# Optimization experiments

Hardware: AMD Instinct MI355X
Metric: run time of the kernel (lower is better)

The kernel has to match this reference:

```python
import jax, jax.numpy as jnp
import numpy as np
import math

DIM = 1024
HEADS = 16
HEAD_DIM = DIM // HEADS
ROT = min(HEAD_DIM, 32)  # rotary_dim
B, S = 2, 1024


def setup_inputs() -> dict:
    key = jax.random.key(0)
    ks = jax.random.split(key, 32)
    lin = lambda k: jax.random.normal(k, (DIM, DIM), jnp.float32) * 0.02
    bias = lambda k: jax.random.normal(k, (DIM,), jnp.float32) * 0.01
    inp = {
        'real': jax.random.normal(ks[0], (B, S, DIM), jnp.float32),
        'imag': jax.random.normal(ks[1], (B, S, DIM), jnp.float32),
        'Wq_r': lin(ks[2]), 'bq_r': bias(ks[3]),
        'Wk_r': lin(ks[4]), 'bk_r': bias(ks[5]),
        'Wv_r': lin(ks[6]), 'bv_r': bias(ks[7]),
        'Wq_i': lin(ks[8]), 'bq_i': bias(ks[9]),
        'Wk_i': lin(ks[10]), 'bk_i': bias(ks[11]),
        'Wv_i': lin(ks[12]), 'bv_i': bias(ks[13]),
        'Wo_r': lin(ks[14]), 'bo_r': bias(ks[15]),
        'Wo_i': lin(ks[16]), 'bo_i': bias(ks[17]),
        'phase_shifts': jax.random.normal(ks[18], (HEADS, HEAD_DIM), jnp.float32) * 0.02,
        'ent': jnp.eye(HEADS, dtype=jnp.float32) + jax.random.normal(ks[19], (HEADS, HEADS), jnp.float32) * 0.01,
        'rot_freqs': (10000.0 ** (-jnp.arange(0, ROT, 2, dtype=jnp.float32) / ROT)),
        'strength': jnp.ones((1,), jnp.float32),
        'temp': jnp.ones((1,), jnp.float32),
    }
    return inp


def _fwd(real, imag, Wq_r, bq_r, Wk_r, bk_r, Wv_r, bv_r,
         Wq_i, bq_i, Wk_i, bk_i, Wv_i, bv_i,
         Wo_r, bo_r, Wo_i, bo_i,
         phase_shifts, ent, rot_freqs, strength, temp):
    b, s, _ = real.shape
    to_heads = lambda t: t.reshape(b, s, HEADS, HEAD_DIM).transpose(0, 2, 1, 3)  # bhsd
    lin = lambda x, W, bb: x @ W + bb

    q_r = to_heads(lin(real, Wq_r, bq_r))
    k_r = to_heads(lin(real, Wk_r, bk_r))
    v_r = to_heads(lin(real, Wv_r, bv_r))
    q_i = to_heads(lin(imag, Wq_i, bq_i))
    k_i = to_heads(lin(imag, Wk_i, bk_i))
    v_i = to_heads(lin(imag, Wv_i, bv_i))

    # rotary on first ROT dims (pairwise rotation)
    pos = jnp.arange(s, dtype=jnp.float32)
    emb = pos[:, None] * rot_freqs[None, :]           # [S, ROT/2]
    cos = jnp.cos(emb)[None, None]                    # [1,1,S,ROT/2]
    sin = jnp.sin(emb)[None, None]

    def rope(t):
        tr = t[..., :ROT].reshape(b, HEADS, s, ROT // 2, 2)
        r0 = tr[..., 0] * cos - tr[..., 1] * sin
        r1 = tr[..., 1] * cos + tr[..., 0] * sin
        rr = jnp.stack([r0, r1], axis=-1).reshape(b, HEADS, s, ROT)
        return jnp.concatenate([rr, t[..., ROT:]], axis=-1)

    q_r, k_r = rope(q_r), rope(k_r)
    q_i, k_i = rope(q_i), rope(k_i)

    # entanglement mixing across heads
    mix = lambda t: jnp.einsum('bhsd,hx->bxsd', t, ent)
    q_r, q_i, k_r, k_i = mix(q_r), mix(q_i), mix(k_r), mix(k_i)

    # per-head phase shift (complex rotation)
    pc = jnp.cos(phase_shifts)[None, :, None, :]      # [1,H,1,D]
    ps = jnp.sin(phase_shifts)[None, :, None, :]
    q_r, q_i = q_r * pc - q_i * ps, q_r * ps + q_i * pc
    k_r, k_i = k_r * pc - k_i * ps, k_r * ps + k_i * pc

    scale = 1.0 / math.sqrt(HEAD_DIM)
    attn_r = (jnp.einsum('bhqd,bhkd->bhqk', q_r, k_r) + jnp.einsum('bhqd,bhkd->bhqk', q_i, k_i)) * scale
    attn_i = (jnp.einsum('bhqd,bhkd->bhqk', q_i, k_r) - jnp.einsum('bhqd,bhkd->bhqk', q_r, k_i)) * scale
    attn_mag = jnp.sqrt(attn_r ** 2 + attn_i ** 2 + 1e-6)

    causal = jnp.triu(jnp.ones((s, s), dtype=bool), k=1)[None, None]
    attn_mag = jnp.where(causal, -jnp.inf, attn_mag)

    t = jnp.maximum(temp, 0.01)
    g = jax.nn.sigmoid(strength)
    attn = jax.nn.softmax(attn_mag * g / t, axis=-1)

    out_r = jnp.einsum('bhqk,bhkd->bhqd', attn, v_r).transpose(0, 2, 1, 3).reshape(b, s, DIM)
    out_i = jnp.einsum('bhqk,bhkd->bhqd', attn, v_i).transpose(0, 2, 1, 3).reshape(b, s, DIM)
    return lin(out_r, Wo_r, bo_r), lin(out_i, Wo_i, bo_i)


def reference(real, imag, Wq_r, bq_r, Wk_r, bk_r, Wv_r, bv_r,
              Wq_i, bq_i, Wk_i, bk_i, Wv_i, bv_i,
              Wo_r, bo_r, Wo_i, bo_i,
              phase_shifts, ent, rot_freqs, strength, temp):
    return _fwd(real, imag, Wq_r, bq_r, Wk_r, bk_r, Wv_r, bv_r,
                Wq_i, bq_i, Wk_i, bk_i, Wv_i, bv_i,
                Wo_r, bo_r, Wo_i, bo_i,
                phase_shifts, ent, rot_freqs, strength, temp)
```

## Files before the change

kernel.cpp:

```cpp
#include <hip/hip_runtime.h>
#include <stdint.h>

typedef unsigned short u16;
typedef __bf16 bf16x8 __attribute__((ext_vector_type(8)));
typedef float f32x4 __attribute__((ext_vector_type(4)));
typedef unsigned int u32x4 __attribute__((ext_vector_type(4)));

__device__ __forceinline__ u16 f2bf(float f) {
  uint32_t u = __float_as_uint(f);
  u += 0x7FFFu + ((u >> 16) & 1u);
  return (u16)(u >> 16);
}
__device__ __forceinline__ float bf2f(u16 h) {
  return __uint_as_float(((uint32_t)h) << 16);
}
__device__ __forceinline__ float fsqrt(float x) {
  float r; asm("v_sqrt_f32 %0, %1" : "=v"(r) : "v"(x)); return r;
}
__device__ __forceinline__ void gld16(const void* g, void* lds) {
  __builtin_amdgcn_global_load_lds(
      (const __attribute__((address_space(1))) uint32_t*)g,
      (__attribute__((address_space(3))) uint32_t*)lds, 16, 0, 0);
}
__device__ __forceinline__ f32x4 mfma16(u32x4 a, u32x4 b, f32x4 c) {
  return __builtin_amdgcn_mfma_f32_16x16x32_bf16(
      __builtin_bit_cast(bf16x8, a), __builtin_bit_cast(bf16x8, b), c, 0, 0, 0);
}

__global__ __launch_bounds__(256) void tables_kernel(const float* __restrict__ rotf,
                                                     const float* __restrict__ phase,
                                                     float* __restrict__ T) {
  int id = blockIdx.x * 256 + threadIdx.x;
  if (id < 16384) {
    int s = id >> 4, jj = id & 15;
    float sn, cs;
    sincosf((float)s * rotf[jj], &sn, &cs);
    T[id] = cs;
    T[16384 + id] = sn;
  } else if (id < 16384 + 1024) {
    int p = id - 16384;
    float sn, cs;
    sincosf(phase[p], &sn, &cs);
    T[32768 + p] = cs;
    T[33792 + p] = sn;
  }
}

__global__ __launch_bounds__(256) void convx_kernel(const float* __restrict__ real,
                                                    const float* __restrict__ imag,
                                                    u16* __restrict__ Xr,
                                                    u16* __restrict__ Xi) {
  int u = blockIdx.x * 256 + threadIdx.x;
  int a = u >> 18;
  int r = u & 262143;
  int m = r >> 7, slot = r & 127;
  const float* src = (a ? imag : real) + (size_t)m * 1024 + slot * 8;
  int slot2 = (slot & ~7) | ((slot ^ m) & 7);
  u16* dst = (a ? Xi : Xr) + (size_t)m * 1024 + slot2 * 8;
  f32x4 v0 = *(const f32x4*)(src);
  f32x4 v1 = *(const f32x4*)(src + 4);
  union { u16 h[8]; u32x4 v; } o;
#pragma unroll
  for (int e = 0; e < 4; ++e) { o.h[e] = f2bf(v0[e]); o.h[4 + e] = f2bf(v1[e]); }
  *(u32x4*)dst = o.v;
}

__global__ __launch_bounds__(256) void convw_kernel(
    const float* __restrict__ w0, const float* __restrict__ w1,
    const float* __restrict__ w2, const float* __restrict__ w3,
    const float* __restrict__ w4, const float* __restrict__ w5,
    const float* __restrict__ w6, const float* __restrict__ w7,
    u16* __restrict__ WtAll) {
  __shared__ float Lt[64][65];
  int z = blockIdx.z;
  const float* W = (z == 0) ? w0 : (z == 1) ? w1 : (z == 2) ? w2 : (z == 3) ? w3
                 : (z == 4) ? w4 : (z == 5) ? w5 : (z == 6) ? w6 : w7;
  u16* Wt = WtAll + (size_t)z * (1024 * 1024);
  int tid = threadIdx.x;
  int n0 = blockIdx.x * 64, k0 = blockIdx.y * 64;
#pragma unroll
  for (int it = 0; it < 4; ++it) {
    int idx = it * 256 + tid;
    int kr = idx >> 4, nc = (idx & 15) * 4;
    f32x4 v = *(const f32x4*)(W + (size_t)(k0 + kr) * 1024 + n0 + nc);
#pragma unroll
    for (int e = 0; e < 4; ++e) Lt[kr][nc + e] = v[e];
  }
  __syncthreads();
#pragma unroll
  for (int it = 0; it < 2; ++it) {
    int idx = it * 256 + tid;
    int nr = idx >> 3, sl = idx & 7;
    union { u16 h[8]; u32x4 v; } o;
#pragma unroll
    for (int e = 0; e < 8; ++e) o.h[e] = f2bf(Lt[sl * 8 + e][nr]);
    int sl2 = sl ^ (nr & 7);
    *(u32x4*)(Wt + (size_t)(n0 + nr) * 1024 + k0 + sl2 * 8) = o.v;
  }
}

__device__ __forceinline__ void gemm128(const u16* __restrict__ A, const u16* __restrict__ W,
                                        const float* __restrict__ bias,
                                        u16* __restrict__ outB, float* __restrict__ outF) {
  __shared__ __align__(16) u16 As[2][128 * 64];
  __shared__ __align__(16) u16 Bs[2][128 * 64];
  int tid = threadIdx.x, l = tid & 63, w = tid >> 6;
  int lr = l & 15, lh = l >> 4;
  int m0 = blockIdx.y * 128, n0 = blockIdx.x * 128;
  int wr = w >> 1, wc = w & 1;
  f32x4 acc[4][4];
#pragma unroll
  for (int mi = 0; mi < 4; ++mi)
#pragma unroll
    for (int ni = 0; ni < 4; ++ni) acc[mi][ni] = f32x4{0.f, 0.f, 0.f, 0.f};

  const u16* aA = A + (size_t)(m0 + w * 8 + (l >> 3)) * 1024 + (l & 7) * 8;
  const u16* aW = W + (size_t)(n0 + w * 8 + (l >> 3)) * 1024 + (l & 7) * 8;
  int ldoff = w * 1024 + l * 16;

  auto stage = [&](int buf, int kt) {
    const u16* pA = aA + kt * 64;
    const u16* pW = aW + kt * 64;
    char* dA = (char*)As[buf] + ldoff;
    char* dB = (char*)Bs[buf] + ldoff;
#pragma unroll
    for (int c = 0; c < 4; ++c) {
      gld16(pA + c * 32768, dA + c * 4096);
      gld16(pW + c * 32768, dB + c * 4096);
    }
  };

  stage(0, 0);

  for (int kt = 0; kt < 16; ++kt) {
    int cur = kt & 1;
    if (kt < 15) {
      stage(cur ^ 1, kt + 1);
      asm volatile("s_waitcnt vmcnt(8)" ::: "memory");
    } else {
      asm volatile("s_waitcnt vmcnt(0)" ::: "memory");
    }
    __builtin_amdgcn_sched_barrier(0);
    asm volatile("s_barrier" ::: "memory");

    const char* cA = (const char*)As[cur];
    const char* cB = (const char*)Bs[cur];
#pragma unroll
    for (int kk = 0; kk < 2; ++kk) {
      u32x4 af[4], bf[4];
#pragma unroll
      for (int mi = 0; mi < 4; ++mi) {
        int row = wr * 64 + mi * 16 + lr;
        af[mi] = *(const u32x4*)(cA + row * 128 +
                                 ((kk * 64 + lh * 16) ^ ((row & 7) << 4)));
      }
#pragma unroll
      for (int ni = 0; ni < 4; ++ni) {
        int row = wc * 64 + ni * 16 + lr;
        bf[ni] = *(const u32x4*)(cB + row * 128 +
                                 ((kk * 64 + lh * 16) ^ ((row & 7) << 4)));
      }
#pragma unroll
      for (int mi = 0; mi < 4; ++mi)
#pragma unroll
        for (int ni = 0; ni < 4; ++ni)
          acc[mi][ni] = mfma16(af[mi], bf[ni], acc[mi][ni]);
    }
    asm volatile("s_barrier" ::: "memory");
  }
#pragma unroll
  for (int ni = 0; ni < 4; ++ni) {
    int col = n0 + wc * 64 + ni * 16 + lr;
    float bv = bias[col];
#pragma unroll
    for (int mi = 0; mi < 4; ++mi)
#pragma unroll
      for (int rr = 0; rr < 4; ++rr) {
        int row = m0 + wr * 64 + mi * 16 + 4 * lh + rr;
        float v = acc[mi][ni][rr] + bv;
        if (outF) outF[(size_t)row * 1024 + col] = v;
        else      outB[(size_t)row * 1024 + col] = f2bf(v);
      }
  }
}

__global__ __launch_bounds__(256) void gemm_proj_kernel(
    const u16* __restrict__ Xr, const u16* __restrict__ Xi, const u16* __restrict__ Wt,
    const float* b0, const float* b1, const float* b2,
    const float* b3, const float* b4, const float* b5,
    u16* __restrict__ qkv) {
  int z = blockIdx.z;
  const u16* A = (z < 3) ? Xr : Xi;
  const u16* W = Wt + (size_t)z * (1024 * 1024);
  const float* bias = (z == 0) ? b0 : (z == 1) ? b1 : (z == 2) ? b2
                    : (z == 3) ? b3 : (z == 4) ? b4 : b5;
  u16* out = qkv + (size_t)z * (2048 * 1024);
  gemm128(A, W, bias, out, nullptr);
}

__global__ __launch_bounds__(256) void gemm_out_kernel(
    const u16* __restrict__ O, const u16* __restrict__ Wt2,
    const float* br, const float* bi, float* __restrict__ dout) {
  int z = blockIdx.z;
  gemm128(O + (size_t)z * (2048 * 1024), Wt2 + (size_t)z * (1024 * 1024),
          z ? bi : br, nullptr, dout + (size_t)z * (2048 * 1024));
}

__global__ __launch_bounds__(256) void transform_kernel(
    const u16* __restrict__ qkv, const float* __restrict__ ent,
    const float* __restrict__ T,
    u16* __restrict__ Qr, u16* __restrict__ Qi, u16* __restrict__ Kr,
    u16* __restrict__ Ki, u16* __restrict__ Vr, u16* __restrict__ Vi) {
  __shared__ float Lqr[16][65], Lqi[16][65], Lkr[16][65], Lki[16][65];
  __shared__ float sent[256];
  int tid = threadIdx.x;
  int bs = blockIdx.x;
  int b = bs >> 10, s = bs & 1023;
  sent[tid] = ent[tid];
  const u16* qr_raw = qkv;
  const u16* kr_raw = qkv + (size_t)1 * 2048 * 1024;
  const u16* vr_raw = qkv + (size_t)2 * 2048 * 1024;
  const u16* qi_raw = qkv + (size_t)3 * 2048 * 1024;
  const u16* ki_raw = qkv + (size_t)4 * 2048 * 1024;
  const u16* vi_raw = qkv + (size_t)5 * 2048 * 1024;
  size_t rowoff = (size_t)bs * 1024;
#pragma unroll
  for (int it = 0; it < 2; ++it) {
    int u = it * 256 + tid;
    int hh = u >> 5, j = u & 31;
    int base = hh * 64 + 2 * j;
    uint32_t aqr = *(const uint32_t*)(qr_raw + rowoff + base);
    uint32_t aqi = *(const uint32_t*)(qi_raw + rowoff + base);
    uint32_t akr = *(const uint32_t*)(kr_raw + rowoff + base);
    uint32_t aki = *(const uint32_t*)(ki_raw + rowoff + base);
    float qr0 = bf2f((u16)aqr), qr1 = bf2f((u16)(aqr >> 16));
    float qi0 = bf2f((u16)aqi), qi1 = bf2f((u16)(aqi >> 16));
    float kr0 = bf2f((u16)akr), kr1 = bf2f((u16)(akr >> 16));
    float ki0 = bf2f((u16)aki), ki1 = bf2f((u16)(aki >> 16));
    if (j < 16) {
      float cs = T[s * 16 + j];
      float sn = T[16384 + s * 16 + j];
      float t0;
      t0 = qr0; qr0 = t0 * cs - qr1 * sn; qr1 = qr1 * cs + t0 * sn;
      t0 = qi0; qi0 = t0 * cs - qi1 * sn; qi1 = qi1 * cs + t0 * sn;
      t0 = kr0; kr0 = t0 * cs - kr1 * sn; kr1 = kr1 * cs + t0 * sn;
      t0 = ki0; ki0 = t0 * cs - ki1 * sn; ki1 = ki1 * cs + t0 * sn;
    }
    int d0 = 2 * j;
    Lqr[hh][d0] = qr0; Lqr[hh][d0 + 1] = qr1;
    Lqi[hh][d0] = qi0; Lqi[hh][d0 + 1] = qi1;
    Lkr[hh][d0] = kr0; Lkr[hh][d0 + 1] = kr1;
    Lki[hh][d0] = ki0; Lki[hh][d0 + 1] = ki1;
  }
  __syncthreads();
#pragma unroll
  for (int it = 0; it < 4; ++it) {
    int u = it * 256 + tid;
    int x = u >> 6, d = u & 63;
    float mqr = 0.f, mqi = 0.f, mkr = 0.f, mki = 0.f;
#pragma unroll
    for (int hh = 0; hh < 16; ++hh) {
      float e = sent[hh * 16 + x];
      mqr += Lqr[hh][d] * e; mqi += Lqi[hh][d] * e;
      mkr += Lkr[hh][d] * e; mki += Lki[hh][d] * e;
    }
    float pc_ = T[32768 + x * 64 + d];
    float ps_ = T[33792 + x * 64 + d];
    float oqr = (mqr * pc_ - mqi * ps_) * 0.125f;
    float oqi = (mqr * ps_ + mqi * pc_) * 0.125f;
    float okr = mkr * pc_ - mki * ps_;
    float oki = mkr * ps_ + mki * pc_;
    size_t obase = ((size_t)(b * 16 + x) * 1024 + s) * 64;
    Qr[obase + d] = f2bf(oqr);
    Qi[obase + d] = f2bf(oqi);
    int dsw = (d & 7) | ((((d >> 3) ^ s) & 7) << 3);
    Kr[obase + dsw] = f2bf(okr);
    Ki[obase + dsw] = f2bf(oki);
  }
  {
    int u = tid;
    int comp = u >> 7, hh = (u >> 3) & 15, sl = u & 7;
    const u16* src = comp ? vi_raw : vr_raw;
    u16* dst = comp ? Vi : Vr;
    u32x4 vv = *(const u32x4*)(src + rowoff + hh * 64 + sl * 8);
    *(u32x4*)(dst + ((size_t)(b * 16 + hh) * 1024 + s) * 64 + sl * 8) = vv;
  }
}

__global__ __launch_bounds__(256) void transv_kernel(const u16* __restrict__ Vr,
                                                     const u16* __restrict__ Vi,
                                                     u16* __restrict__ VTr,
                                                     u16* __restrict__ VTi) {
  int bid = blockIdx.x;
  int comp = bid >> 9, bh = (bid >> 4) & 31, t = bid & 15;
  const u16* src = (comp ? Vi : Vr) + ((size_t)bh * 1024 + t * 64) * 64;
  u16* dst = (comp ? VTi : VTr) + (size_t)bh * 65536;
  __shared__ __align__(16) u16 Lt[64][72];
  int tid = threadIdx.x;
#pragma unroll
  for (int it = 0; it < 2; ++it) {
    int i = it * 256 + tid;
    int r = i >> 3, sl = i & 7;
    *(u32x4*)(&Lt[r][sl * 8]) = *(const u32x4*)(src + r * 64 + sl * 8);
  }
  __syncthreads();
#pragma unroll
  for (int it = 0; it < 2; ++it) {
    int i = it * 256 + tid;
    int d = i >> 3, sl = i & 7;
    union { u16 h[8]; u32x4 v; } o;
#pragma unroll
    for (int e = 0; e < 8; ++e) o.h[e] = Lt[sl * 8 + e][d];
    int sl2 = sl ^ (d & 7);
    *(u32x4*)(dst + (size_t)d * 1024 + t * 64 + sl2 * 8) = o.v;
  }
}

__global__ __launch_bounds__(256) void attn_kernel(
    const u16* __restrict__ Qr, const u16* __restrict__ Qi,
    const u16* __restrict__ Kr, const u16* __restrict__ Ki,
    const u16* __restrict__ VTr, const u16* __restrict__ VTi,
    const float* __restrict__ strength, const float* __restrict__ temp,
    u16* __restrict__ por0, u16* __restrict__ por1,
    u16* __restrict__ por2, u16* __restrict__ por3,
    u16* __restrict__ poi0, u16* __restrict__ poi1,
    u16* __restrict__ poi2, u16* __restrict__ poi3,
    float* __restrict__ Pm, float* __restrict__ Pl) {
  __shared__ __align__(16) u16 smem[20480];
  char* sb = (char*)smem;
  const int PO = 32768;
  int tid = threadIdx.x, l = tid & 63, w = tid >> 6;
  int lr = l & 15, lh = l >> 4;
  int id = blockIdx.x;
  int x = id & 7, j = id >> 3;
  int bh = x + 8 * (j & 3);
  int cc = j >> 2;
  int qb, sp;
  if (cc < 16)      { qb = 15 - (cc >> 2); sp = cc & 3; }
  else if (cc < 28) { int r = cc - 16; int q3 = r / 3; qb = 11 - q3; sp = r - 3 * q3; }
  else if (cc < 36) { int r = cc - 28; qb = 7 - (r >> 1); sp = r & 1; }
  else              { qb = 39 - cc; sp = 0; }
  int q0 = qb * 64;
  int t0 = sp * 4, t1 = min(qb + 1, t0 + 4);
  int b = bh >> 4; (void)b;
  u16* POr = (sp == 0) ? por0 : (sp == 1) ? por1 : (sp == 2) ? por2 : por3;
  u16* POi = (sp == 0) ? poi0 : (sp == 1) ? poi1 : (sp == 2) ? poi2 : poi3;

  float g = 1.f / (1.f + __expf(-strength[0]));
  float tt = fmaxf(temp[0], 0.01f);
  float gt = g / tt;

  size_t qbase = ((size_t)bh * 1024 + q0 + w * 16 + lr) * 64 + lh * 8;
  u32x4 qrF[2], qiF[2], nqrF[2];
#pragma unroll
  for (int kk = 0; kk < 2; ++kk) {
    qrF[kk] = *(const u32x4*)(Qr + qbase + kk * 32);
    qiF[kk] = *(const u32x4*)(Qi + qbase + kk * 32);
    nqrF[kk] = qrF[kk] ^ 0x80008000u;
  }
  f32x4 o_r[4], o_i[4];
#pragma unroll
  for (int n = 0; n < 4; ++n) { o_r[n] = f32x4{0,0,0,0}; o_i[n] = f32x4{0,0,0,0}; }
  float m_run[4], l_run[4];
#pragma unroll
  for (int rr = 0; rr < 4; ++rr) { m_run[rr] = -__builtin_inff(); l_run[rr] = 0.f; }

  const u16* gK = ((w == 1) ? Ki : Kr) + ((size_t)bh * 1024 + t0 * 64) * 64 + l * 8;
  char* ldK = sb + (w == 1 ? 8192 : 0);
  const u16* gV = ((w == 3) ? VTi : VTr) + (size_t)bh * 65536 + t0 * 64 +
                  (l >> 3) * 1024 + (l & 7) * 8;
  char* ldV = sb + (w == 3 ? 24576 : 16384);

  for (int t = t0; t < t1; ++t) {
    if (w < 2) {
#pragma unroll
      for (int c = 0; c < 8; ++c) gld16(gK + c * 512, ldK + c * 1024);
      gK += 4096;
    } else {
#pragma unroll
      for (int c = 0; c < 8; ++c) gld16(gV + c * 8192, ldV + c * 1024);
      gV += 64;
    }
    __syncthreads();

    f32x4 sr[4], si[4];
#pragma unroll
    for (int n = 0; n < 4; ++n) { sr[n] = f32x4{0,0,0,0}; si[n] = f32x4{0,0,0,0}; }
#pragma unroll
    for (int kk = 0; kk < 2; ++kk) {
#pragma unroll
      for (int n = 0; n < 4; ++n) {
        int kv = n * 16 + lr;
        int xoff = (kk * 64 + lh * 16) ^ ((kv & 7) << 4);
        u32x4 fkr = *(const u32x4*)(sb + kv * 128 + xoff);
        u32x4 fki = *(const u32x4*)(sb + 8192 + kv * 128 + xoff);
        sr[n] = mfma16(qrF[kk], fkr, sr[n]);
        sr[n] = mfma16(qiF[kk], fki, sr[n]);
        si[n] = mfma16(qiF[kk], fkr, si[n]);
        si[n] = mfma16(nqrF[kk], fki, si[n]);
      }
    }

    float pl_[4][4], pm[4];
#pragma unroll
    for (int rr = 0; rr < 4; ++rr) pm[rr] = -__builtin_inff();
    bool diag = (t == qb);
#pragma unroll
    for (int n = 0; n < 4; ++n)
#pragma unroll
      for (int rr = 0; rr < 4; ++rr) {
        float a = sr[n][rr], ci = si[n][rr];
        float mag = fsqrt(a * a + ci * ci + 1e-6f) * gt;
        if (diag) {
          if (n * 16 + lr > w * 16 + 4 * lh + rr) mag = -__builtin_inff();
        }
        pl_[n][rr] = mag;
        pm[rr] = fmaxf(pm[rr], mag);
      }
#pragma unroll
    for (int mk = 1; mk <= 8; mk <<= 1)
#pragma unroll
      for (int rr = 0; rr < 4; ++rr)
        pm[rr] = fmaxf(pm[rr], __shfl_xor(pm[rr], mk));

    bool defer = true;
#pragma unroll
    for (int rr = 0; rr < 4; ++rr) defer = defer && (pm[rr] - m_run[rr] <= 8.f);
    bool noresc = __all(defer ? 1 : 0);
    float fr[4];
    if (!noresc) {
#pragma unroll
      for (int rr = 0; rr < 4; ++rr) {
        float mnew = fmaxf(m_run[rr], pm[rr]);
        fr[rr] = __expf(m_run[rr] - mnew);
        m_run[rr] = mnew;
      }
    }
    float rs[4];
#pragma unroll
    for (int rr = 0; rr < 4; ++rr) rs[rr] = 0.f;
#pragma unroll
    for (int n = 0; n < 4; ++n)
#pragma unroll
      for (int rr = 0; rr < 4; ++rr) {
        float p = __expf(pl_[n][rr] - m_run[rr]);
        pl_[n][rr] = p;
        rs[rr] += p;
      }
#pragma unroll
    for (int mk = 1; mk <= 8; mk <<= 1)
#pragma unroll
      for (int rr = 0; rr < 4; ++rr)
        rs[rr] += __shfl_xor(rs[rr], mk);
    if (!noresc) {
#pragma unroll
      for (int rr = 0; rr < 4; ++rr) l_run[rr] = l_run[rr] * fr[rr] + rs[rr];
#pragma unroll
      for (int n = 0; n < 4; ++n)
#pragma unroll
        for (int rr = 0; rr < 4; ++rr) { o_r[n][rr] *= fr[rr]; o_i[n][rr] *= fr[rr]; }
    } else {
#pragma unroll
      for (int rr = 0; rr < 4; ++rr) l_run[rr] += rs[rr];
    }

    char* pw = sb + PO + w * 2048;
#pragma unroll
    for (int n = 0; n < 4; ++n)
#pragma unroll
      for (int rr = 0; rr < 4; ++rr) {
        int row = 4 * lh + rr, col = n * 16 + lr;
        int by = row * 128 + ((col & 7) * 2) + ((((col >> 3) ^ row) & 7) << 4);
        *(u16*)(pw + by) = f2bf(pl_[n][rr]);
      }
    u32x4 pf[2];
#pragma unroll
    for (int kk = 0; kk < 2; ++kk)
      pf[kk] = *(const u32x4*)(pw + lr * 128 + ((kk * 64 + lh * 16) ^ ((lr & 7) << 4)));
#pragma unroll
    for (int kk = 0; kk < 2; ++kk)
#pragma unroll
      for (int n = 0; n < 4; ++n) {
        int dl = n * 16 + lr;
        int xoff = (kk * 64 + lh * 16) ^ ((dl & 7) << 4);
        u32x4 fvr = *(const u32x4*)(sb + 16384 + dl * 128 + xoff);
        u32x4 fvi = *(const u32x4*)(sb + 24576 + dl * 128 + xoff);
        o_r[n] = mfma16(pf[kk], fvr, o_r[n]);
        o_i[n] = mfma16(pf[kk], fvi, o_i[n]);
      }
    __syncthreads();
  }

  size_t pbase = ((size_t)bh * 1024 + q0 + w * 16 + 4 * lh) * 64;
#pragma unroll
  for (int n = 0; n < 4; ++n)
#pragma unroll
    for (int rr = 0; rr < 4; ++rr) {
      POr[pbase + rr * 64 + n * 16 + lr] = f2bf(o_r[n][rr]);
      POi[pbase + rr * 64 + n * 16 + lr] = f2bf(o_i[n][rr]);
    }
  if (lr == 0) {
    size_t mbase = (size_t)sp * 32768 + (size_t)bh * 1024 + q0 + w * 16 + 4 * lh;
#pragma unroll
    for (int rr = 0; rr < 4; ++rr) {
      Pm[mbase + rr] = m_run[rr];
      Pl[mbase + rr] = l_run[rr];
    }
  }
}

__global__ __launch_bounds__(256) void combine_kernel(
    const u16* __restrict__ por0, const u16* __restrict__ por1,
    const u16* __restrict__ por2, const u16* __restrict__ por3,
    const u16* __restrict__ poi0, const u16* __restrict__ poi1,
    const u16* __restrict__ poi2, const u16* __restrict__ poi3,
    const float* __restrict__ Pm, const float* __restrict__ Pl,
    u16* __restrict__ Or, u16* __restrict__ Oi) {
  int bid = blockIdx.x;
  int bh = bid >> 4, rg = bid & 15;
  int b = bh >> 4, h = bh & 15;
  int ns = (rg >> 2) + 1;
  int tid = threadIdx.x;
  int row = tid >> 2, q = tid & 3;
  int s = rg * 64 + row;
  size_t ro = (size_t)bh * 1024 + s;
  const u16* PR[4] = {por0, por1, por2, por3};
  const u16* PI[4] = {poi0, poi1, poi2, poi3};
  float msp[4], lsp[4], csw[4];
  float M = -__builtin_inff();
#pragma unroll
  for (int sp = 0; sp < 4; ++sp) {
    if (sp < ns) {
      msp[sp] = Pm[ro + (size_t)sp * 32768];
      lsp[sp] = Pl[ro + (size_t)sp * 32768];
      M = fmaxf(M, msp[sp]);
    }
  }
  float lt = 0.f;
#pragma unroll
  for (int sp = 0; sp < 4; ++sp) {
    if (sp < ns) { csw[sp] = __expf(msp[sp] - M); lt += lsp[sp] * csw[sp]; }
    else csw[sp] = 0.f;
  }
  float inv = 1.f / lt;
#pragma unroll
  for (int sp = 0; sp < 4; ++sp) csw[sp] *= inv;
  size_t obase = ro * 64;
#pragma unroll
  for (int g = 0; g < 2; ++g) {
    int d = q * 16 + g * 8;
    float accr[8], acci[8];
#pragma unroll
    for (int e = 0; e < 8; ++e) { accr[e] = 0.f; acci[e] = 0.f; }
#pragma unroll
    for (int sp = 0; sp < 4; ++sp) {
      if (sp < ns) {
        union { u16 h[8]; u32x4 v; } ar, ai;
        ar.v = *(const u32x4*)(PR[sp] + obase + d);
        ai.v = *(const u32x4*)(PI[sp] + obase + d);
#pragma unroll
        for (int e = 0; e < 8; ++e) {
          accr[e] += csw[sp] * bf2f(ar.h[e]);
          acci[e] += csw[sp] * bf2f(ai.h[e]);
        }
      }
    }
    union { u16 h[8]; u32x4 v; } outr, outi;
#pragma unroll
    for (int e = 0; e < 8; ++e) { outr.h[e] = f2bf(accr[e]); outi.h[e] = f2bf(acci[e]); }
    int slot2 = (d >> 3) ^ (s & 7);
    size_t oo = ((size_t)b * 1024 + s) * 1024 + h * 64 + slot2 * 8;
    *(u32x4*)(Or + oo) = outr.v;
    *(u32x4*)(Oi + oo) = outi.v;
  }
}

extern "C" void kernel_launch(void* const* d_in, const int* in_sizes, int n_in,
                              void* d_out, int out_size, void* d_ws, size_t ws_size,
                              hipStream_t stream) {
  (void)in_sizes; (void)n_in; (void)out_size; (void)ws_size;
  const float* real = (const float*)d_in[0];
  const float* imag = (const float*)d_in[1];
  const float* bq_r = (const float*)d_in[3];
  const float* bk_r = (const float*)d_in[5];
  const float* bv_r = (const float*)d_in[7];
  const float* bq_i = (const float*)d_in[9];
  const float* bk_i = (const float*)d_in[11];
  const float* bv_i = (const float*)d_in[13];
  const float* bo_r = (const float*)d_in[15];
  const float* bo_i = (const float*)d_in[17];
  const float* phase = (const float*)d_in[18];
  const float* ent = (const float*)d_in[19];
  const float* rotf = (const float*)d_in[20];
  const float* strength = (const float*)d_in[21];
  const float* temp = (const float*)d_in[22];

  u16* ws = (u16*)d_ws;
  const size_t M1 = 1024 * 1024, M2 = 2048 * 1024;
  u16* Xr  = ws;
  u16* Xi  = Xr + M2;
  u16* Wt  = Xi + M2;
  u16* qkv = Wt + 8 * M1;
  u16* Qr  = qkv + 6 * M2;
  u16* Qi  = Qr + M2;
  u16* Kr  = Qi + M2;
  u16* Ki  = Kr + M2;
  u16* Vr  = Ki + M2;
  u16* Vi  = Vr + M2;
  u16* VTr = Vi + M2;
  u16* VTi = VTr + M2;
  u16* Or  = VTi + M2;
  u16* Oi  = Or + M2;
  u16* por0 = qkv;
  u16* por1 = qkv + M2;
  u16* por2 = qkv + 2 * M2;
  u16* por3 = qkv + 3 * M2;
  u16* poi0 = qkv + 4 * M2;
  u16* poi1 = qkv + 5 * M2;
  u16* poi2 = Vr;
  u16* poi3 = Vi;
  float* Pm = (float*)Xr;
  float* Pl = Pm + 131072;
  float* TBL = (float*)Oi;

  tables_kernel<<<68, 256, 0, stream>>>(rotf, phase, TBL);
  convx_kernel<<<2048, 256, 0, stream>>>(real, imag, Xr, Xi);
  convw_kernel<<<dim3(16, 16, 8), 256, 0, stream>>>(
      (const float*)d_in[2],  (const float*)d_in[4],  (const float*)d_in[6],
      (const float*)d_in[8],  (const float*)d_in[10], (const float*)d_in[12],
      (const float*)d_in[14], (const float*)d_in[16], Wt);
  gemm_proj_kernel<<<dim3(8, 16, 6), 256, 0, stream>>>(Xr, Xi, Wt, bq_r, bk_r, bv_r,
                                                       bq_i, bk_i, bv_i, qkv);
  transform_kernel<<<2048, 256, 0, stream>>>(qkv, ent, TBL, Qr, Qi, Kr, Ki, Vr, Vi);
  transv_kernel<<<1024, 256, 0, stream>>>(Vr, Vi, VTr, VTi);
  attn_kernel<<<1280, 256, 0, stream>>>(Qr, Qi, Kr, Ki, VTr, VTi, strength, temp,
                                        por0, por1, por2, por3,
                                        poi0, poi1, poi2, poi3, Pm, Pl);
  combine_kernel<<<512, 256, 0, stream>>>(por0, por1, por2, por3,
                                          poi0, poi1, poi2, poi3, Pm, Pl, Or, Oi);
  gemm_out_kernel<<<dim3(8, 16, 2), 256, 0, stream>>>(Or, Wt + 6 * M1, bo_r, bo_i,
                                                      (float*)d_out);
}
```

Before: 151.3 us.

## Load K and V fragments directly from global memory instead of staging through LDS

The attention kernel no longer stages K and V tiles into shared memory with cooperative global_load_lds and block barriers. Each wave now loads its MFMA operand fragments for K and transposed V straight from global memory into registers. The XOR swizzle applied when writing K and VT is removed because LDS bank conflicts no longer matter for them. This drops both __syncthreads per tile and cuts LDS use, but each of the four waves now fetches the full K/V tile separately, quadrupling global/L2 traffic, and it raises register pressure with no prefetch overlap.

```diff
diff --git a/kernel.cpp b/kernel.cpp
--- a/kernel.cpp
+++ b/kernel.cpp
@@ -273,9 +273,8 @@
     size_t obase = ((size_t)(b * 16 + x) * 1024 + s) * 64;
     Qr[obase + d] = f2bf(oqr);
     Qi[obase + d] = f2bf(oqi);
-    int dsw = (d & 7) | ((((d >> 3) ^ s) & 7) << 3);
-    Kr[obase + dsw] = f2bf(okr);
-    Ki[obase + dsw] = f2bf(oki);
+    Kr[obase + d] = f2bf(okr);
+    Ki[obase + d] = f2bf(oki);
   }
   {
     int u = tid;
@@ -311,8 +310,7 @@
     union { u16 h[8]; u32x4 v; } o;
 #pragma unroll
     for (int e = 0; e < 8; ++e) o.h[e] = Lt[sl * 8 + e][d];
-    int sl2 = sl ^ (d & 7);
-    *(u32x4*)(dst + (size_t)d * 1024 + t * 64 + sl2 * 8) = o.v;
+    *(u32x4*)(dst + (size_t)d * 1024 + t * 64 + sl * 8) = o.v;
   }
 }
 
@@ -326,9 +324,8 @@
     u16* __restrict__ poi0, u16* __restrict__ poi1,
     u16* __restrict__ poi2, u16* __restrict__ poi3,
     float* __restrict__ Pm, float* __restrict__ Pl) {
-  __shared__ __align__(16) u16 smem[20480];
+  __shared__ __align__(16) u16 smem[4096];
   char* sb = (char*)smem;
-  const int PO = 32768;
   int tid = threadIdx.x, l = tid & 63, w = tid >> 6;
   int lr = l & 15, lh = l >> 4;
   int id = blockIdx.x;
@@ -365,23 +362,31 @@
 #pragma unroll
   for (int rr = 0; rr < 4; ++rr) { m_run[rr] = -__builtin_inff(); l_run[rr] = 0.f; }
 
-  const u16* gK = ((w == 1) ? Ki : Kr) + ((size_t)bh * 1024 + t0 * 64) * 64 + l * 8;
-  char* ldK = sb + (w == 1 ? 8192 : 0);
-  const u16* gV = ((w == 3) ? VTi : VTr) + (size_t)bh * 65536 + t0 * 64 +
-                  (l >> 3) * 1024 + (l & 7) * 8;
-  char* ldV = sb + (w == 3 ? 24576 : 16384);
+  const u16* Kr_b = Kr + (size_t)bh * 65536;
+  const u16* Ki_b = Ki + (size_t)bh * 65536;
+  const u16* Vr_b = VTr + (size_t)bh * 65536;
+  const u16* Vi_b = VTi + (size_t)bh * 65536;
+  char* pw = sb + w * 2048;
 
   for (int t = t0; t < t1; ++t) {
-    if (w < 2) {
-#pragma unroll
-      for (int c = 0; c < 8; ++c) gld16(gK + c * 512, ldK + c * 1024);
-      gK += 4096;
-    } else {
-#pragma unroll
-      for (int c = 0; c < 8; ++c) gld16(gV + c * 8192, ldV + c * 1024);
-      gV += 64;
-    }
-    __syncthreads();
+    const u16* Kt_r = Kr_b + t * 4096;
+    const u16* Kt_i = Ki_b + t * 4096;
+    u32x4 fkr[2][4], fki[2][4];
+#pragma unroll
+    for (int kk = 0; kk < 2; ++kk)
+#pragma unroll
+      for (int n = 0; n < 4; ++n) {
+        int off = (n * 16 + lr) * 64 + kk * 32 + lh * 8;
+        fkr[kk][n] = *(const u32x4*)(Kt_r + off);
+        fki[kk][n] = *(const u32x4*)(Kt_i + off);
+      }
+    u32x4 fvr0[4], fvi0[4];
+#pragma unroll
+    for (int n = 0; n < 4; ++n) {
+      size_t voff = (size_t)(n * 16 + lr) * 1024 + t * 64 + lh * 8;
+      fvr0[n] = *(const u32x4*)(Vr_b + voff);
+      fvi0[n] = *(const u32x4*)(Vi_b + voff);
+    }
 
     f32x4 sr[4], si[4];
 #pragma unroll
@@ -390,14 +395,10 @@
     for (int kk = 0; kk < 2; ++kk) {
 #pragma unroll
       for (int n = 0; n < 4; ++n) {
-        int kv = n * 16 + lr;
-        int xoff = (kk * 64 + lh * 16) ^ ((kv & 7) << 4);
-        u32x4 fkr = *(const u32x4*)(sb + kv * 128 + xoff);
-        u32x4 fki = *(const u32x4*)(sb + 8192 + kv * 128 + xoff);
-        sr[n] = mfma16(qrF[kk], fkr, sr[n]);
-        sr[n] = mfma16(qiF[kk], fki, sr[n]);
-        si[n] = mfma16(qiF[kk], fkr, si[n]);
-        si[n] = mfma16(nqrF[kk], fki, si[n]);
+        sr[n] = mfma16(qrF[kk], fkr[kk][n], sr[n]);
+        sr[n] = mfma16(qiF[kk], fki[kk][n], sr[n]);
+        si[n] = mfma16(qiF[kk], fkr[kk][n], si[n]);
+        si[n] = mfma16(nqrF[kk], fki[kk][n], si[n]);
       }
     }
 
@@ -464,7 +465,6 @@
       for (int rr = 0; rr < 4; ++rr) l_run[rr] += rs[rr];
     }
 
-    char* pw = sb + PO + w * 2048;
 #pragma unroll
     for (int n = 0; n < 4; ++n)
 #pragma unroll
@@ -477,18 +477,24 @@
 #pragma unroll
     for (int kk = 0; kk < 2; ++kk)
       pf[kk] = *(const u32x4*)(pw + lr * 128 + ((kk * 64 + lh * 16) ^ ((lr & 7) << 4)));
-#pragma unroll
-    for (int kk = 0; kk < 2; ++kk)
-#pragma unroll
-      for (int n = 0; n < 4; ++n) {
-        int dl = n * 16 + lr;
-        int xoff = (kk * 64 + lh * 16) ^ ((dl & 7) << 4);
-        u32x4 fvr = *(const u32x4*)(sb + 16384 + dl * 128 + xoff);
-        u32x4 fvi = *(const u32x4*)(sb + 24576 + dl * 128 + xoff);
-        o_r[n] = mfma16(pf[kk], fvr, o_r[n]);
-        o_i[n] = mfma16(pf[kk], fvi, o_i[n]);
-      }
-    __syncthreads();
+
+    u32x4 fvr1[4], fvi1[4];
+#pragma unroll
+    for (int n = 0; n < 4; ++n) {
+      size_t voff = (size_t)(n * 16 + lr) * 1024 + t * 64 + 32 + lh * 8;
+      fvr1[n] = *(const u32x4*)(Vr_b + voff);
+      fvi1[n] = *(const u32x4*)(Vi_b + voff);
+    }
+#pragma unroll
+    for (int n = 0; n < 4; ++n) {
+      o_r[n] = mfma16(pf[0], fvr0[n], o_r[n]);
+      o_i[n] = mfma16(pf[0], fvi0[n], o_i[n]);
+    }
+#pragma unroll
+    for (int n = 0; n < 4; ++n) {
+      o_r[n] = mfma16(pf[1], fvr1[n], o_r[n]);
+      o_i[n] = mfma16(pf[1], fvi1[n], o_i[n]);
+    }
   }
 
   size_t pbase = ((size_t)bh * 1024 + q0 + w * 16 + 4 * lh) * 64;
```

Measured after the change: 191.8 us. +26.8%, slower.
